# Optimization experiments

Hardware: AMD Instinct MI355X
Metric: run time of the kernel (lower is better)

Reference implementation:

```python
import jax, jax.numpy as jnp
import numpy as np

B, S, D, H = 2, 2048, 2048, 16
HD = D // H


def setup_inputs() -> dict:
    key = jax.random.key(0)
    ks = jax.random.split(key, 9)
    scale = 0.02
    return {
        "x": jax.random.normal(ks[0], (B, S, D), dtype=jnp.float32),
        "wq_w": jax.random.normal(ks[1], (D, D), dtype=jnp.float32) * scale,
        "wq_b": jnp.zeros((D,), dtype=jnp.float32),
        "wk_w": jax.random.normal(ks[2], (D, D), dtype=jnp.float32) * scale,
        "wk_b": jnp.zeros((D,), dtype=jnp.float32),
        "wv_w": jax.random.normal(ks[3], (D, D), dtype=jnp.float32) * scale,
        "wv_b": jnp.zeros((D,), dtype=jnp.float32),
        "wo_w": jax.random.normal(ks[4], (D, D), dtype=jnp.float32) * scale,
        "wo_b": jnp.zeros((D,), dtype=jnp.float32),
    }


def reference(x, wq_w, wq_b, wk_w, wk_b, wv_w, wv_b, wo_w, wo_b):
    # torch Linear: y = x @ W.T + b
    q = x @ wq_w.T + wq_b  # [B,S,D]
    k = x @ wk_w.T + wk_b
    v = x @ wv_w.T + wv_b
    # [B,S,D] -> [B,H,S,HD]
    q = q.reshape(B, S, H, HD).transpose(0, 2, 1, 3)
    k = k.reshape(B, S, H, HD).transpose(0, 2, 1, 3)
    v = v.reshape(B, S, H, HD).transpose(0, 2, 1, 3)
    # scores [B,H,S,S], scaled by sqrt(d_dim) as in the original (not head_dim)
    scores = jnp.einsum("bhid,bhjd->bhij", q, k) / np.float32(np.sqrt(D))
    # faithful reproduction of the module's triu/transpose masking:
    m = jnp.swapaxes(jnp.triu(scores), -2, -1)  # lower-tri, zeros elsewhere
    p = jax.nn.softmax(m, axis=-2)              # softmax over dim=-2, zeros included
    a = jnp.swapaxes(jnp.triu(p), -2, -1)       # [B,H,S,S]
    attn = jnp.einsum("bhij,bhjd->bhid", a, v)  # [B,H,S,HD]
    concat = attn.transpose(0, 2, 1, 3).reshape(B, S, D)
    return concat @ wo_w.T + wo_b
```

## Files before the change

### kernel.cpp

```cpp
#include <hip/hip_runtime.h>

#define BB 2
#define SS 2048
#define DD 2048
#define HH 16
#define HDIM 128
#define MTOK (BB*SS)
#define BHH (BB*HH)
#define NCHUNK 16
#define QKN (2*DD)

typedef __attribute__((ext_vector_type(8))) __bf16 bf16x8;
typedef __attribute__((ext_vector_type(4))) float f32x4;
typedef __attribute__((ext_vector_type(8))) int i32x8;

__device__ __forceinline__ unsigned short f2bf(float f) {
  unsigned u = __float_as_uint(f);
  u += 0x7FFFu + ((u >> 16) & 1u);
  return (unsigned short)(u >> 16);
}
__device__ __forceinline__ float bf2f(unsigned short s) {
  return __uint_as_float(((unsigned)s) << 16);
}
__device__ __forceinline__ unsigned char f2e4m3(float f) {
  int pk = __builtin_amdgcn_cvt_pk_fp8_f32(f, f, 0, false);
  return (unsigned char)(pk & 0xFF);
}

#define GLOAD_LDS16(src, dst)                                                   \
  __builtin_amdgcn_global_load_lds(                                             \
      (const void __attribute__((address_space(1)))*)(src),                     \
      (void __attribute__((address_space(3)))*)(dst), 16, 0, 0)

__global__ void cvt_x_dual(const float* __restrict__ in,
                           unsigned short* __restrict__ outb,
                           unsigned int* __restrict__ out8, int n4) {
  int i = blockIdx.x * blockDim.x + threadIdx.x;
  if (i < n4) {
    float4 v = ((const float4*)in)[i];
    ushort4 o;
    o.x = f2bf(v.x); o.y = f2bf(v.y); o.z = f2bf(v.z); o.w = f2bf(v.w);
    ((ushort4*)outb)[i] = o;
    int p0 = __builtin_amdgcn_cvt_pk_fp8_f32(v.x, v.y, 0, false);
    int p1 = __builtin_amdgcn_cvt_pk_fp8_f32(v.z, v.w, 0, false);
    out8[i] = (unsigned)(p0 & 0xFFFF) | ((unsigned)(p1 & 0xFFFF) << 16);
  }
}

__global__ void cvt_wqk8(const float* __restrict__ a, const float* __restrict__ b,
                         unsigned int* __restrict__ out) {
  int i = blockIdx.x * blockDim.x + threadIdx.x;
  int sel = i >> 20, r = i & 0xFFFFF;
  const float* src = sel == 0 ? a : b;
  float4 v = ((const float4*)src)[r];
  int p0 = __builtin_amdgcn_cvt_pk_fp8_f32(v.x, v.y, 0, false);
  int p1 = __builtin_amdgcn_cvt_pk_fp8_f32(v.z, v.w, 0, false);
  out[i] = (unsigned)(p0 & 0xFFFF) | ((unsigned)(p1 & 0xFFFF) << 16);
}

__global__ void cvt_w2bf(const float* __restrict__ a, const float* __restrict__ b,
                         unsigned short* __restrict__ out) {
  int i = blockIdx.x * blockDim.x + threadIdx.x;
  int sel = i >> 20, r = i & 0xFFFFF;
  const float* src = sel == 0 ? a : b;
  float4 v = ((const float4*)src)[r];
  ushort4 o;
  o.x = f2bf(v.x); o.y = f2bf(v.y); o.z = f2bf(v.z); o.w = f2bf(v.w);
  ((ushort4*)out)[i] = o;
}

__global__ void concat2(const float* __restrict__ a, const float* __restrict__ b,
                        float* __restrict__ out) {
  int i = blockIdx.x * blockDim.x + threadIdx.x;
  if (i < DD) { out[i] = a[i]; out[DD + i] = b[i]; }
}

template <bool OUT_BF16>
__global__ __launch_bounds__(256, 2) void gemm_bt(
    const __bf16* __restrict__ A, const __bf16* __restrict__ W,
    const float* __restrict__ bias, void* __restrict__ Cout,
    int M, int N, int K) {
  __shared__ __bf16 lA[128 * 32];
  __shared__ __bf16 lB[128 * 32];
  const int t = threadIdx.x;
  const int lane = t & 63, wave = t >> 6;
  const int quad = lane >> 4, l16 = lane & 15;
  const int m0 = blockIdx.y * 128, n0 = blockIdx.x * 128;
  const int wm = (wave & 1) * 64, wn = (wave >> 1) * 64;

  f32x4 acc[4][4] = {};

  for (int k0 = 0; k0 < K; k0 += 32) {
#pragma unroll
    for (int c = 0; c < 2; ++c) {
      int lin = c * 256 + t;
      int row = lin >> 2;
      int col = (lin & 3) * 8;
      const __bf16* srcA = A + (size_t)(m0 + row) * K + k0 + col;
      const __bf16* srcB = W + (size_t)(n0 + row) * K + k0 + col;
      GLOAD_LDS16(srcA, &lA[(c * 256 + wave * 64) * 8]);
      GLOAD_LDS16(srcB, &lB[(c * 256 + wave * 64) * 8]);
    }
    __syncthreads();
    bf16x8 af[4], bfr[4];
#pragma unroll
    for (int mt = 0; mt < 4; ++mt)
      af[mt] = *(const bf16x8*)&lA[(wm + mt * 16 + l16) * 32 + quad * 8];
#pragma unroll
    for (int nt = 0; nt < 4; ++nt)
      bfr[nt] = *(const bf16x8*)&lB[(wn + nt * 16 + l16) * 32 + quad * 8];
#pragma unroll
    for (int mt = 0; mt < 4; ++mt)
#pragma unroll
      for (int nt = 0; nt < 4; ++nt)
        acc[mt][nt] = __builtin_amdgcn_mfma_f32_16x16x32_bf16(af[mt], bfr[nt],
                                                              acc[mt][nt], 0, 0, 0);
    __syncthreads();
  }

#pragma unroll
  for (int mt = 0; mt < 4; ++mt) {
#pragma unroll
    for (int nt = 0; nt < 4; ++nt) {
      int col = n0 + wn + nt * 16 + l16;
      float bv = bias[col];
#pragma unroll
      for (int r = 0; r < 4; ++r) {
        int row = m0 + wm + mt * 16 + quad * 4 + r;
        float v = acc[mt][nt][r] + bv;
        if constexpr (OUT_BF16)
          ((unsigned short*)Cout)[(size_t)row * N + col] = f2bf(v);
        else
          ((float*)Cout)[(size_t)row * N + col] = v;
      }
    }
  }
}

__global__ __launch_bounds__(256, 2) void gemm_qk_fp8(
    const unsigned char* __restrict__ A8, const unsigned char* __restrict__ W8,
    const float* __restrict__ bias, unsigned char* __restrict__ Cout,
    int M, int N, int K) {
  __shared__ unsigned char lA[128 * 128];
  __shared__ unsigned char lB[128 * 128];
  const int t = threadIdx.x;
  const int lane = t & 63, wave = t >> 6;
  const int quad = lane >> 4, l16 = lane & 15;
  const int m0 = blockIdx.y * 128, n0 = blockIdx.x * 128;
  const int wm = (wave & 1) * 64, wn = (wave >> 1) * 64;

  f32x4 acc[4][4] = {};

  for (int k0 = 0; k0 < K; k0 += 128) {
#pragma unroll
    for (int c = 0; c < 4; ++c) {
      int lin = c * 256 + t;
      int row = lin >> 3;
      int ch = lin & 7;
      const unsigned char* srcA = A8 + (size_t)(m0 + row) * K + k0 + ch * 16;
      const unsigned char* srcB = W8 + (size_t)(n0 + row) * K + k0 + ch * 16;
      GLOAD_LDS16(srcA, &lA[(c * 256 + wave * 64) * 16]);
      GLOAD_LDS16(srcB, &lB[(c * 256 + wave * 64) * 16]);
    }
    __syncthreads();
    i32x8 af[4];
#pragma unroll
    for (int mt = 0; mt < 4; ++mt)
      af[mt] = *(const i32x8*)&lA[(wm + mt * 16 + l16) * 128 + quad * 32];
#pragma unroll
    for (int nt = 0; nt < 4; ++nt) {
      i32x8 bfr = *(const i32x8*)&lB[(wn + nt * 16 + l16) * 128 + quad * 32];
#pragma unroll
      for (int mt = 0; mt < 4; ++mt)
        acc[mt][nt] = __builtin_amdgcn_mfma_scale_f32_16x16x128_f8f6f4(
            af[mt], bfr, acc[mt][nt], 0 , 0 ,
            0, 127 , 0, 127 );
    }
    __syncthreads();
  }

#pragma unroll
  for (int mt = 0; mt < 4; ++mt) {
#pragma unroll
    for (int nt = 0; nt < 4; ++nt) {
      int col = n0 + wn + nt * 16 + l16;
      float bv = bias[col];
#pragma unroll
      for (int r = 0; r < 4; ++r) {
        int row = m0 + wm + mt * 16 + quad * 4 + r;
        Cout[(size_t)row * N + col] = f2e4m3(acc[mt][nt][r] + bv);
      }
    }
  }
}

__global__ __launch_bounds__(256, 2) void qk_rowsum8(
    const unsigned char* __restrict__ q8, const unsigned char* __restrict__ k8,
    float* __restrict__ denom, float* __restrict__ diag) {
  __shared__ unsigned char lK[4 * 128 * 32];
  const int t = threadIdx.x;
  const int lane = t & 63, wave = t >> 6;
  const int quad = lane >> 4, l16 = lane & 15;
  const int bh = blockIdx.y;
  const int b = bh >> 4, h = bh & 15;
  const float scale = 0.02209708691207961f;

#pragma unroll
  for (int sub = 0; sub < 2; ++sub) {
    const int tile = (sub == 0) ? (int)blockIdx.x : 31 - (int)blockIdx.x;
    const int i0 = tile * 64;
    const int rowg = i0 + wave * 16;

    long long af[4];
    const unsigned char* qbase =
        q8 + (size_t)(b * SS + rowg + l16) * QKN + h * HDIM;
#pragma unroll
    for (int ks = 0; ks < 4; ++ks)
      af[ks] = *(const long long*)(qbase + ks * 32 + quad * 8);

    float rowsum[4] = {0.f, 0.f, 0.f, 0.f};
    float diagv[4] = {0.f, 0.f, 0.f, 0.f};

    for (int j0 = i0 & ~127; j0 < SS; j0 += 128) {
#pragma unroll
      for (int c = 0; c < 4; ++c) {
        int L = c * 256 + t;
        int ks = L >> 8;
        int rem = L & 255;
        int row = rem >> 1;
        int c2 = rem & 1;
        const unsigned char* src =
            k8 + (size_t)(b * SS + j0 + row) * QKN + h * HDIM + ks * 32 + c2 * 16;
        GLOAD_LDS16(src, &lK[(c * 256 + wave * 64) * 16]);
      }
      __syncthreads();
#pragma unroll
      for (int nt = 0; nt < 8; ++nt) {
        f32x4 acc = {0.f, 0.f, 0.f, 0.f};
#pragma unroll
        for (int ks = 0; ks < 4; ++ks) {
          long long bfr =
              *(const long long*)&lK[ks * 4096 + (nt * 16 + l16) * 32 + quad * 8];
          acc = __builtin_amdgcn_mfma_f32_16x16x32_fp8_fp8(af[ks], bfr, acc, 0, 0, 0);
        }
        int colg = j0 + nt * 16 + l16;
#pragma unroll
        for (int r = 0; r < 4; ++r) {
          int rg = rowg + quad * 4 + r;
          if (colg >= rg) {
            float e = __expf(acc[r] * scale);
            rowsum[r] += e;
            if (colg == rg) diagv[r] = e;
          }
        }
      }
      __syncthreads();
    }

#pragma unroll
    for (int r = 0; r < 4; ++r) {
      float s = rowsum[r], d = diagv[r];
#pragma unroll
      for (int off = 1; off < 16; off <<= 1) {
        s += __shfl_xor(s, off, 64);
        d += __shfl_xor(d, off, 64);
      }
      if (l16 == 0) {
        int rg = rowg + quad * 4 + r;
        denom[bh * SS + rg] = (float)rg + s;
        diag[bh * SS + rg] = d;
      }
    }
  }
}

__global__ void scan_pass1(const __bf16* __restrict__ v0,
                           float* __restrict__ csum) {
  int blk = blockIdx.x;
  int bh = blk >> 4, c = blk & 15;
  int b = bh >> 4, h = bh & 15;
  int t = threadIdx.x;
  int rs = t >> 4, dg = t & 15;
  const unsigned short* base = (const unsigned short*)v0 +
      (size_t)(b * SS + c * 128 + rs * 8) * DD + h * HDIM + dg * 8;
  float s[8] = {0.f, 0.f, 0.f, 0.f, 0.f, 0.f, 0.f, 0.f};
#pragma unroll
  for (int i = 0; i < 8; ++i) {
    uint4 u = *(const uint4*)(base + (size_t)i * DD);
    const unsigned short* us = (const unsigned short*)&u;
#pragma unroll
    for (int j = 0; j < 8; ++j) s[j] += bf2f(us[j]);
  }
  __shared__ float red[16 * 128];
#pragma unroll
  for (int j = 0; j < 8; ++j) red[rs * 128 + dg * 8 + j] = s[j];
  __syncthreads();
  for (int st = 8; st >= 1; st >>= 1) {
    if (rs < st) {
#pragma unroll
      for (int j = 0; j < 8; ++j)
        red[rs * 128 + dg * 8 + j] += red[(rs + st) * 128 + dg * 8 + j];
    }
    __syncthreads();
  }
  if (rs == 0) {
#pragma unroll
    for (int j = 0; j < 8; ++j)
      csum[(size_t)blk * 128 + dg * 8 + j] = red[dg * 8 + j];
  }
}

__global__ void scan_pass2(const __bf16* __restrict__ v0,
                           const float* __restrict__ csum,
                           const float* __restrict__ denom,
                           const float* __restrict__ diag,
                           unsigned short* __restrict__ ctx) {
  int blk = blockIdx.x;
  int bh = blk >> 4, c = blk & 15;
  int b = bh >> 4, h = bh & 15;
  int t = threadIdx.x;
  int rs = t >> 4, dg = t & 15;
  const unsigned short* vbase = (const unsigned short*)v0 +
      (size_t)(b * SS + c * 128 + rs * 8) * DD + h * HDIM + dg * 8;
  float vrow[8][8];
  float ls[8] = {0.f, 0.f, 0.f, 0.f, 0.f, 0.f, 0.f, 0.f};
#pragma unroll
  for (int i = 0; i < 8; ++i) {
    uint4 u = *(const uint4*)(vbase + (size_t)i * DD);
    const unsigned short* us = (const unsigned short*)&u;
#pragma unroll
    for (int j = 0; j < 8; ++j) {
      vrow[i][j] = bf2f(us[j]);
      ls[j] += vrow[i][j];
    }
  }
  __shared__ float red[16 * 128];
#pragma unroll
  for (int j = 0; j < 8; ++j) red[rs * 128 + dg * 8 + j] = ls[j];
  __syncthreads();

  float pre[8] = {0.f, 0.f, 0.f, 0.f, 0.f, 0.f, 0.f, 0.f};
  for (int cc = 0; cc < c; ++cc) {
    const float* cp = csum + (size_t)(bh * 16 + cc) * 128 + dg * 8;
#pragma unroll
    for (int j = 0; j < 8; ++j) pre[j] += cp[j];
  }
  for (int ss2 = 0; ss2 < rs; ++ss2) {
#pragma unroll
    for (int j = 0; j < 8; ++j) pre[j] += red[ss2 * 128 + dg * 8 + j];
  }

  int row0 = c * 128 + rs * 8;
  unsigned short* obase =
      ctx + (size_t)(b * SS + row0) * DD + h * HDIM + dg * 8;
  const float* dn = denom + bh * SS + row0;
  const float* dgp = diag + bh * SS + row0;
#pragma unroll
  for (int i = 0; i < 8; ++i) {
    float inv = 1.0f / dn[i];
    float dv = dgp[i];
    unsigned short o[8];
#pragma unroll
    for (int j = 0; j < 8; ++j) {
      float val = (pre[j] + dv * vrow[i][j]) * inv;
      o[j] = f2bf(val);
      pre[j] += vrow[i][j];
    }
    *(uint4*)(obase + (size_t)i * DD) = *(const uint4*)o;
  }
}

extern "C" void kernel_launch(void* const* d_in, const int* in_sizes, int n_in,
                              void* d_out, int out_size, void* d_ws, size_t ws_size,
                              hipStream_t stream) {
  (void)in_sizes; (void)n_in; (void)out_size; (void)ws_size;
  const float* x    = (const float*)d_in[0];
  const float* wq_w = (const float*)d_in[1];
  const float* wq_b = (const float*)d_in[2];
  const float* wk_w = (const float*)d_in[3];
  const float* wk_b = (const float*)d_in[4];
  const float* wv_w = (const float*)d_in[5];
  const float* wv_b = (const float*)d_in[6];
  const float* wo_w = (const float*)d_in[7];
  const float* wo_b = (const float*)d_in[8];

  char* ws = (char*)d_ws;
  size_t off = 0;
  auto alloc = [&](size_t bytes) {
    char* p = ws + off;
    off += (bytes + 255) & ~(size_t)255;
    return p;
  };
  unsigned short* xb   = (unsigned short*)alloc((size_t)MTOK * DD * 2);
  unsigned char*  x8   = (unsigned char*)alloc((size_t)MTOK * DD);
  unsigned char*  wqk8 = (unsigned char*)alloc((size_t)2 * DD * DD);
  unsigned short* wvo  = (unsigned short*)alloc((size_t)2 * DD * DD * 2);
  unsigned char*  qk8  = (unsigned char*)alloc((size_t)MTOK * QKN);
  unsigned short* v    = (unsigned short*)alloc((size_t)MTOK * DD * 2);
  unsigned short* ctx  = (unsigned short*)alloc((size_t)MTOK * DD * 2);
  float* biasqk = (float*)alloc((size_t)2 * DD * 4);
  float* denom  = (float*)alloc((size_t)BHH * SS * 4);
  float* diag   = (float*)alloc((size_t)BHH * SS * 4);
  float* csum   = (float*)alloc((size_t)BHH * NCHUNK * 128 * 4);

  {
    int n4 = MTOK * DD / 4;
    cvt_x_dual<<<n4 / 256, 256, 0, stream>>>(x, xb, (unsigned int*)x8, n4);
    cvt_wqk8<<<(2 << 20) / 256, 256, 0, stream>>>(wq_w, wk_w, (unsigned int*)wqk8);
    cvt_w2bf<<<(2 << 20) / 256, 256, 0, stream>>>(wv_w, wo_w, wvo);
    concat2<<<(DD + 255) / 256, 256, 0, stream>>>(wq_b, wk_b, biasqk);
  }

  gemm_qk_fp8<<<dim3(QKN / 128, MTOK / 128), 256, 0, stream>>>(
      x8, wqk8, biasqk, qk8, MTOK, QKN, DD);

  gemm_bt<true><<<dim3(DD / 128, MTOK / 128), 256, 0, stream>>>(
      (const __bf16*)xb, (const __bf16*)wvo, wv_b, v, MTOK, DD, DD);

  qk_rowsum8<<<dim3(16, BHH), 256, 0, stream>>>(
      qk8,
      qk8 + DD,
      denom, diag);

  scan_pass1<<<BHH * NCHUNK, 256, 0, stream>>>((const __bf16*)v, csum);
  scan_pass2<<<BHH * NCHUNK, 256, 0, stream>>>((const __bf16*)v, csum,
                                               denom, diag, ctx);

  gemm_bt<false><<<dim3(DD / 128, MTOK / 128), 256, 0, stream>>>(
      (const __bf16*)ctx, (const __bf16*)(wvo + (size_t)DD * DD), wo_b,
      d_out, MTOK, DD, DD);
}
```

Before: 367.5 us.

## Rebalance QK rowsum with split segments, MX fp8 MFMA and swizzled LDS

Rewrites the causal QK row-sum kernel to use the 16x16x128 scaled fp8 MFMA with a full 128-wide K tile in LDS, XOR-swizzled to avoid bank conflicts. Work is split into 32 blocks per head: long query tiles are divided into two segments whose partial sums go to separate denominator buffers (denomA/denomB), which scan_pass2 adds together. The aim is better load balance, higher occupancy (launch bounds 4) and fewer MFMA issues. It adds an extra buffer and an LDS cross-wave reduction, and masking is now applied only on the diagonal tile.

```diff
diff --git a/kernel.cpp b/kernel.cpp
--- a/kernel.cpp
+++ b/kernel.cpp
@@ -173,8 +173,7 @@
 #pragma unroll
       for (int mt = 0; mt < 4; ++mt)
         acc[mt][nt] = __builtin_amdgcn_mfma_scale_f32_16x16x128_f8f6f4(
-            af[mt], bfr, acc[mt][nt], 0 , 0 ,
-            0, 127 , 0, 127 );
+            af[mt], bfr, acc[mt][nt], 0, 0, 0, 127, 0, 127);
     }
     __syncthreads();
   }
@@ -194,83 +193,115 @@
   }
 }
 
-__global__ __launch_bounds__(256, 2) void qk_rowsum8(
+__global__ __launch_bounds__(256, 4) void qk_rowsum_mx(
     const unsigned char* __restrict__ q8, const unsigned char* __restrict__ k8,
-    float* __restrict__ denom, float* __restrict__ diag) {
-  __shared__ unsigned char lK[4 * 128 * 32];
+    float* __restrict__ denomA, float* __restrict__ denomB,
+    float* __restrict__ diag) {
+  __shared__ unsigned char lK[128 * 128];
+  __shared__ float lred[2 * 256];
   const int t = threadIdx.x;
   const int lane = t & 63, wave = t >> 6;
   const int quad = lane >> 4, l16 = lane & 15;
   const int bh = blockIdx.y;
   const int b = bh >> 4, h = bh & 15;
-  const float scale = 0.02209708691207961f;
-
-#pragma unroll
-  for (int sub = 0; sub < 2; ++sub) {
-    const int tile = (sub == 0) ? (int)blockIdx.x : 31 - (int)blockIdx.x;
-    const int i0 = tile * 64;
-    const int rowg = i0 + wave * 16;
-
-    long long af[4];
-    const unsigned char* qbase =
-        q8 + (size_t)(b * SS + rowg + l16) * QKN + h * HDIM;
-#pragma unroll
-    for (int ks = 0; ks < 4; ++ks)
-      af[ks] = *(const long long*)(qbase + ks * 32 + quad * 8);
-
-    float rowsum[4] = {0.f, 0.f, 0.f, 0.f};
-    float diagv[4] = {0.f, 0.f, 0.f, 0.f};
-
-    for (int j0 = i0 & ~127; j0 < SS; j0 += 128) {
+  const int p = blockIdx.x & 15, hf = blockIdx.x >> 4;
+  const float SL2E = 0.03188233603f;
+
+  const int nseg = hf ? 2 : 1;
+  for (int si = 0; si < nseg; ++si) {
+    int q, jt0, cnt, mode;
+    bool dg;
+    if (hf == 0)      { q = p;      jt0 = p >> 1;       cnt = 9;             dg = true;  mode = 1; }
+    else if (si == 0) { q = p;      jt0 = (p >> 1) + 9; cnt = 7 - (p >> 1);  dg = false; mode = 2; }
+    else              { q = 31 - p; jt0 = q >> 1;       cnt = 16 - (q >> 1); dg = true;  mode = 5; }
+
+    i32x8 af[4];
+#pragma unroll
+    for (int mt = 0; mt < 4; ++mt)
+      af[mt] = *(const i32x8*)(q8 + (size_t)(b * SS + q * 64 + mt * 16 + l16) * QKN
+                               + h * HDIM + quad * 32);
+
+    float rs[4][4] = {};
+    float dv[4][4] = {};
+
+    for (int jt = jt0; jt < jt0 + cnt; ++jt) {
+      const int j0 = jt * 128;
 #pragma unroll
       for (int c = 0; c < 4; ++c) {
         int L = c * 256 + t;
-        int ks = L >> 8;
-        int rem = L & 255;
-        int row = rem >> 1;
-        int c2 = rem & 1;
-        const unsigned char* src =
-            k8 + (size_t)(b * SS + j0 + row) * QKN + h * HDIM + ks * 32 + c2 * 16;
+        int row = L >> 3, ch = L & 7;
+        const unsigned char* src = k8 + (size_t)(b * SS + j0 + row) * QKN
+                                   + h * HDIM + ((ch ^ (row & 7)) * 16);
         GLOAD_LDS16(src, &lK[(c * 256 + wave * 64) * 16]);
       }
       __syncthreads();
-#pragma unroll
-      for (int nt = 0; nt < 8; ++nt) {
-        f32x4 acc = {0.f, 0.f, 0.f, 0.f};
-#pragma unroll
-        for (int ks = 0; ks < 4; ++ks) {
-          long long bfr =
-              *(const long long*)&lK[ks * 4096 + (nt * 16 + l16) * 32 + quad * 8];
-          acc = __builtin_amdgcn_mfma_f32_16x16x32_fp8_fp8(af[ks], bfr, acc, 0, 0, 0);
+      const bool masked = dg && (jt == jt0);
+#pragma unroll
+      for (int ntl = 0; ntl < 2; ++ntl) {
+        int jrow = (wave * 2 + ntl) * 16 + l16;
+        uint4 lo = *(const uint4*)&lK[jrow * 128 + (((quad * 2) ^ (jrow & 7)) * 16)];
+        uint4 hi = *(const uint4*)&lK[jrow * 128 + (((quad * 2 + 1) ^ (jrow & 7)) * 16)];
+        i32x8 bfr;
+        bfr[0] = lo.x; bfr[1] = lo.y; bfr[2] = lo.z; bfr[3] = lo.w;
+        bfr[4] = hi.x; bfr[5] = hi.y; bfr[6] = hi.z; bfr[7] = hi.w;
+        f32x4 sacc[4];
+#pragma unroll
+        for (int mt = 0; mt < 4; ++mt) {
+          f32x4 z = {0.f, 0.f, 0.f, 0.f};
+          sacc[mt] = __builtin_amdgcn_mfma_scale_f32_16x16x128_f8f6f4(
+              af[mt], bfr, z, 0, 0, 0, 127, 0, 127);
         }
-        int colg = j0 + nt * 16 + l16;
-#pragma unroll
-        for (int r = 0; r < 4; ++r) {
-          int rg = rowg + quad * 4 + r;
-          if (colg >= rg) {
-            float e = __expf(acc[r] * scale);
-            rowsum[r] += e;
-            if (colg == rg) diagv[r] = e;
-          }
+        int colg = j0 + jrow;
+        if (masked) {
+#pragma unroll
+          for (int mt = 0; mt < 4; ++mt)
+#pragma unroll
+            for (int r = 0; r < 4; ++r) {
+              int rg = q * 64 + mt * 16 + quad * 4 + r;
+              float e = exp2f(sacc[mt][r] * SL2E);
+              if (colg >= rg) rs[mt][r] += e;
+              if (colg == rg) dv[mt][r] = e;
+            }
+        } else {
+#pragma unroll
+          for (int mt = 0; mt < 4; ++mt)
+#pragma unroll
+            for (int r = 0; r < 4; ++r)
+              rs[mt][r] += exp2f(sacc[mt][r] * SL2E);
         }
       }
       __syncthreads();
     }
 
 #pragma unroll
-    for (int r = 0; r < 4; ++r) {
-      float s = rowsum[r], d = diagv[r];
-#pragma unroll
-      for (int off = 1; off < 16; off <<= 1) {
-        s += __shfl_xor(s, off, 64);
-        d += __shfl_xor(d, off, 64);
-      }
-      if (l16 == 0) {
-        int rg = rowg + quad * 4 + r;
-        denom[bh * SS + rg] = (float)rg + s;
-        diag[bh * SS + rg] = d;
-      }
-    }
+    for (int mt = 0; mt < 4; ++mt)
+#pragma unroll
+      for (int r = 0; r < 4; ++r) {
+        float s = rs[mt][r], d = dv[mt][r];
+#pragma unroll
+        for (int off = 1; off < 16; off <<= 1) {
+          s += __shfl_xor(s, off, 64);
+          d += __shfl_xor(d, off, 64);
+        }
+        if (l16 == 0) {
+          int rl = mt * 16 + quad * 4 + r;
+          lred[wave * 64 + rl] = s;
+          lred[256 + wave * 64 + rl] = d;
+        }
+      }
+    __syncthreads();
+    if (t < 64) {
+      float tot = lred[t] + lred[64 + t] + lred[128 + t] + lred[192 + t];
+      float dtot = lred[256 + t] + lred[320 + t] + lred[384 + t] + lred[448 + t];
+      int rg = q * 64 + t;
+      if (mode & 1) {
+        denomA[bh * SS + rg] = (float)rg + tot;
+        diag[bh * SS + rg] = dtot;
+      }
+      if (mode & 2) denomB[bh * SS + rg] = tot;
+      if (mode & 4) denomB[bh * SS + rg] = 0.f;
+    }
+    __syncthreads();
   }
 }
 
@@ -312,7 +343,8 @@
 
 __global__ void scan_pass2(const __bf16* __restrict__ v0,
                            const float* __restrict__ csum,
-                           const float* __restrict__ denom,
+                           const float* __restrict__ denomA,
+                           const float* __restrict__ denomB,
                            const float* __restrict__ diag,
                            unsigned short* __restrict__ ctx) {
   int blk = blockIdx.x;
@@ -353,16 +385,17 @@
   int row0 = c * 128 + rs * 8;
   unsigned short* obase =
       ctx + (size_t)(b * SS + row0) * DD + h * HDIM + dg * 8;
-  const float* dn = denom + bh * SS + row0;
+  const float* dnA = denomA + bh * SS + row0;
+  const float* dnB = denomB + bh * SS + row0;
   const float* dgp = diag + bh * SS + row0;
 #pragma unroll
   for (int i = 0; i < 8; ++i) {
-    float inv = 1.0f / dn[i];
-    float dv = dgp[i];
+    float inv = 1.0f / (dnA[i] + dnB[i]);
+    float dvv = dgp[i];
     unsigned short o[8];
 #pragma unroll
     for (int j = 0; j < 8; ++j) {
-      float val = (pre[j] + dv * vrow[i][j]) * inv;
+      float val = (pre[j] + dvv * vrow[i][j]) * inv;
       o[j] = f2bf(val);
       pre[j] += vrow[i][j];
     }
@@ -399,7 +432,8 @@
   unsigned short* v    = (unsigned short*)alloc((size_t)MTOK * DD * 2);
   unsigned short* ctx  = (unsigned short*)alloc((size_t)MTOK * DD * 2);
   float* biasqk = (float*)alloc((size_t)2 * DD * 4);
-  float* denom  = (float*)alloc((size_t)BHH * SS * 4);
+  float* denomA = (float*)alloc((size_t)BHH * SS * 4);
+  float* denomB = (float*)alloc((size_t)BHH * SS * 4);
   float* diag   = (float*)alloc((size_t)BHH * SS * 4);
   float* csum   = (float*)alloc((size_t)BHH * NCHUNK * 128 * 4);
 
@@ -417,14 +451,14 @@
   gemm_bt<true><<<dim3(DD / 128, MTOK / 128), 256, 0, stream>>>(
       (const __bf16*)xb, (const __bf16*)wvo, wv_b, v, MTOK, DD, DD);
 
-  qk_rowsum8<<<dim3(16, BHH), 256, 0, stream>>>(
+  qk_rowsum_mx<<<dim3(32, BHH), 256, 0, stream>>>(
       qk8,
       qk8 + DD,
-      denom, diag);
+      denomA, denomB, diag);
 
   scan_pass1<<<BHH * NCHUNK, 256, 0, stream>>>((const __bf16*)v, csum);
   scan_pass2<<<BHH * NCHUNK, 256, 0, stream>>>((const __bf16*)v, csum,
-                                               denom, diag, ctx);
+                                               denomA, denomB, diag, ctx);
 
   gemm_bt<false><<<dim3(DD / 128, MTOK / 128), 256, 0, stream>>>(
       (const __bf16*)ctx, (const __bf16*)(wvo + (size_t)DD * DD), wo_b,
```

Result: no change. 367.9 us (+0.1%).
